# Performance work log

Hardware: AMD Instinct MI355X
Metric: run time of the kernel (lower is better)

The kernel has to match this reference:

```python
import jax, jax.numpy as jnp
import numpy as np

DECAY = 0.99
EPS = 1e-05
B, T, DIM, N_EMBED = 64, 1024, 256, 1024


def setup_inputs() -> dict:
    key = jax.random.key(0)
    k1, k2 = jax.random.split(key, 2)
    input_ = jax.random.normal(k1, (B, T, DIM), dtype=jnp.float32)
    embed = jax.random.normal(k2, (DIM, N_EMBED), dtype=jnp.float32)  # buffer 'embed'
    cluster_size = jnp.zeros((N_EMBED,), dtype=jnp.float32)           # buffer 'cluster_size'
    embed_avg = embed.copy()                                          # buffer 'embed_avg'
    return {"input_": input_, "embed": embed, "cluster_size": cluster_size, "embed_avg": embed_avg}


def reference(input_, embed, cluster_size, embed_avg):
    n_embed = embed.shape[1]
    flatten = input_.reshape(-1, embed.shape[0])  # [N, dim]
    dist = (jnp.sum(flatten * flatten, axis=-1, keepdims=True)
            - 2.0 * flatten @ embed
            + jnp.sum(embed * embed, axis=0, keepdims=True))
    embed_ind = jnp.argmin(dist, axis=1)  # (-dist).max(1) == argmin(dist)
    quantize = jnp.take(embed.T, embed_ind, axis=0).reshape(input_.shape)

    # training-mode EMA codebook update (buffers are detached in torch)
    # embed_onehot_sum = onehot.sum(0); embed_sum = flatten.T @ onehot
    # implemented via segment_sum (same math, no NxK one-hot materialized)
    ones = jnp.ones((flatten.shape[0],), dtype=flatten.dtype)
    embed_onehot_sum = jax.ops.segment_sum(ones, embed_ind, num_segments=n_embed)
    embed_sum = jax.ops.segment_sum(flatten, embed_ind, num_segments=n_embed).T  # [dim, n_embed]

    new_cluster_size = cluster_size * DECAY + (1.0 - DECAY) * embed_onehot_sum
    # NOTE: original code applies .mul_(decay) TWICE to embed_avg -> decay**2 (faithful)
    new_embed_avg = embed_avg * (DECAY * DECAY) + (1.0 - DECAY) * embed_sum
    n = jnp.sum(new_cluster_size)
    cs = (new_cluster_size + EPS) / (n + n_embed * EPS) * n
    new_embed = new_embed_avg / cs[None, :]

    diff = jnp.mean((jax.lax.stop_gradient(quantize) - input_) ** 2)
    quantize_st = input_ + jax.lax.stop_gradient(quantize - input_)
    return quantize_st, diff, embed_ind, new_cluster_size, new_embed_avg, new_embed
```

## Files before the change

kernel.cpp:

```cpp
#include <hip/hip_runtime.h>
#include <float.h>

#define DECAY 0.99f
#define EPS 1e-5f
#define NROWS 65536
#define DIM 256
#define NEMB 1024
#define CH 64
#define MAXSUB 2048

typedef _Float16 f16;
typedef _Float16 half8 __attribute__((ext_vector_type(8)));
typedef float f32x4 __attribute__((ext_vector_type(4)));

__global__ __launch_bounds__(256) void k_enorm(const float* __restrict__ embed,
                                               float* __restrict__ enorm2,
                                               int* __restrict__ counts) {
    int kk = threadIdx.x & 63;
    int dg = threadIdx.x >> 6;
    int k  = blockIdx.x * 64 + kk;
    float s = 0.f;
    for (int d = dg; d < DIM; d += 4) {
        float v = embed[(size_t)d * NEMB + k];
        s = fmaf(v, v, s);
    }
    __shared__ float red[4][64];
    red[dg][kk] = s;
    __syncthreads();
    if (dg == 0) enorm2[k] = red[0][kk] + red[1][kk] + red[2][kk] + red[3][kk];
    int gt = blockIdx.x * 256 + threadIdx.x;
    if (gt < NEMB) counts[gt] = 0;
}

__global__ __launch_bounds__(256) void k_transpose(const float* __restrict__ embed,
                                                   float* __restrict__ embedT) {
    __shared__ float tile[32][33];
    int k0 = blockIdx.x * 32, d0 = blockIdx.y * 32;
    int tx = threadIdx.x, ty = threadIdx.y;
#pragma unroll
    for (int i = 0; i < 4; i++)
        tile[ty + 8 * i][tx] = embed[(size_t)(d0 + ty + 8 * i) * NEMB + k0 + tx];
    __syncthreads();
#pragma unroll
    for (int i = 0; i < 4; i++)
        embedT[(size_t)(k0 + ty + 8 * i) * DIM + d0 + tx] = tile[tx][ty + 8 * i];
}

__global__ __launch_bounds__(256) void k_esplit(const float* __restrict__ embed,
                                                f16* __restrict__ ehlT) {
    __shared__ float tile[32][33];
    int c0 = blockIdx.x * 32, d0 = blockIdx.y * 32;
    int tx = threadIdx.x, ty = threadIdx.y;
#pragma unroll
    for (int i = 0; i < 4; i++)
        tile[ty + 8 * i][tx] = embed[(size_t)(d0 + ty + 8 * i) * NEMB + c0 + tx];
    __syncthreads();
#pragma unroll
    for (int i = 0; i < 4; i++) {
        int c = c0 + ty + 8 * i;
        int d = d0 + tx;
        float v = tile[tx][ty + 8 * i];
        f16 h = (f16)v;
        f16 l = (f16)(v - (float)h);
        ehlT[(size_t)c * 512 + d]       = h;
        ehlT[(size_t)c * 512 + 256 + d] = l;
    }
}

#define LDS_A  0
#define LDS_B  131072
#define LDS_SZ 147456

__global__ __launch_bounds__(512, 2) void k_argmin_mfma(const float* __restrict__ input,
                                                        const f16* __restrict__ ehlT,
                                                        const float* __restrict__ enorm2,
                                                        int* __restrict__ ind,
                                                        float* __restrict__ out_ind) {
    __shared__ char lds[LDS_SZ];
    const int tid  = threadIdx.x;
    const int lane = tid & 63;
    const int w    = tid >> 6;
    const int wr   = w >> 2;
    const int wc   = w & 3;
    const int rb   = blockIdx.x * 128;
    const int l15  = lane & 15;
    const int lkh  = lane >> 4;
    const int swa  = (l15 & 7) << 4;
    const int swb  = ((l15 >> 1) & 3) << 4;

#pragma unroll
    for (int it8 = 0; it8 < 4; it8++) {
        int task = tid + 512 * it8;
        int row = task >> 4, ch = task & 15;
        const float4* g = (const float4*)(input + (size_t)(rb + row) * DIM + ch * 16);
        float fv[16];
        *(float4*)(fv + 0)  = g[0];
        *(float4*)(fv + 4)  = g[1];
        *(float4*)(fv + 8)  = g[2];
        *(float4*)(fv + 12) = g[3];
        half8 hh[2], llv[2];
#pragma unroll
        for (int u = 0; u < 2; u++)
#pragma unroll
            for (int e = 0; e < 8; e++) {
                float x = fv[u * 8 + e];
                f16 h = (f16)x;
                hh[u][e]  = h;
                llv[u][e] = (f16)(x - (float)h);
            }
        int rbase = row * 1024;
        int sw = (row & 7) << 4;
        *(half8*)(lds + LDS_A + rbase + (((ch * 2    ) * 16) ^ sw)) = hh[0];
        *(half8*)(lds + LDS_A + rbase + (((ch * 2 + 1) * 16) ^ sw)) = hh[1];
        *(half8*)(lds + LDS_A + rbase + (((32 + ch * 2) * 16) ^ sw)) = llv[0];
        *(half8*)(lds + LDS_A + rbase + (((33 + ch * 2) * 16) ^ sw)) = llv[1];
    }

#pragma unroll
    for (int u = 0; u < 2; u++) {
        int g = tid + 512 * u;
        int col = g >> 2, s = g & 3;
        half8 h = *(const half8*)(ehlT + (size_t)col * 512 + s * 8);
        *(half8*)(lds + LDS_B + col * 64 + ((s * 16) ^ (((col >> 1) & 3) << 4))) = h;
    }
    __syncthreads();

    float bv[16];
    int   bi[16];
#pragma unroll
    for (int q = 0; q < 16; q++) { bv[q] = FLT_MAX; bi[q] = 0x7fffffff; }

    for (int ct = 0; ct < 4; ct++) {
        const int cb = ct * 256;
        f32x4 acc[4][4];
#pragma unroll
        for (int fr = 0; fr < 4; fr++)
#pragma unroll
            for (int fc = 0; fc < 4; fc++) acc[fr][fc] = (f32x4){0.f, 0.f, 0.f, 0.f};

        for (int kt = 0; kt < 24; kt++) {
            const int it = ct * 24 + kt;
            const bool hn = (it < 95);
            float4 nb0, nb1;
            int wa0 = 0, wa1 = 0;
            if (hn) {
                int itn = it + 1;
                int ct2 = itn / 24;
                int kt2 = itn - ct2 * 24;
                int seg2 = kt2 >> 3, kq2 = kt2 & 7;
                int koff2 = ((seg2 == 2) ? 256 : 0) + kq2 * 32;
                int cb2 = ct2 * 256;
                int g0 = tid, col0 = g0 >> 2, s0 = g0 & 3;
                nb0 = *(const float4*)(ehlT + (size_t)(cb2 + col0) * 512 + koff2 + s0 * 8);
                wa0 = col0 * 64 + ((s0 * 16) ^ (((col0 >> 1) & 3) << 4));
                int g1 = tid + 512, col1 = g1 >> 2, s1 = g1 & 3;
                nb1 = *(const float4*)(ehlT + (size_t)(cb2 + col1) * 512 + koff2 + s1 * 8);
                wa1 = col1 * 64 + ((s1 * 16) ^ (((col1 >> 1) & 3) << 4));
            }
            const int seg = kt >> 3, kq = kt & 7;
            const int abase = ((seg == 1) ? 32 : 0) + kq * 4;
            const int jslot = abase + lkh;
            half8 af[4], bf[4];
#pragma unroll
            for (int f = 0; f < 4; f++) {
                int row = wr * 64 + f * 16 + l15;
                af[f] = *(const half8*)(lds + LDS_A + row * 1024 + ((jslot * 16) ^ swa));
            }
#pragma unroll
            for (int f = 0; f < 4; f++) {
                int col = wc * 64 + f * 16 + l15;
                bf[f] = *(const half8*)(lds + LDS_B + col * 64 + ((lkh * 16) ^ swb));
            }
#pragma unroll
            for (int fr = 0; fr < 4; fr++)
#pragma unroll
                for (int fc = 0; fc < 4; fc++)
                    acc[fr][fc] = __builtin_amdgcn_mfma_f32_16x16x32_f16(
                        af[fr], bf[fc], acc[fr][fc], 0, 0, 0);
            if (kt == 23) {
#pragma unroll
                for (int fc = 0; fc < 4; fc++) {
                    int col = cb + wc * 64 + fc * 16 + l15;
                    float e2 = enorm2[col];
#pragma unroll
                    for (int fr = 0; fr < 4; fr++)
#pragma unroll
                        for (int r = 0; r < 4; r++) {
                            float s = fmaf(-2.f, acc[fr][fc][r], e2);
                            int q = fr * 4 + r;
                            if (s < bv[q]) { bv[q] = s; bi[q] = col; }
                        }
                }
            }
            __syncthreads();
            if (hn) {
                *(half8*)(lds + LDS_B + wa0) = *(half8*)&nb0;
                *(half8*)(lds + LDS_B + wa1) = *(half8*)&nb1;
            }
            __syncthreads();
        }
    }

#pragma unroll
    for (int q = 0; q < 16; q++) {
        float v = bv[q]; int i = bi[q];
#pragma unroll
        for (int m = 1; m <= 8; m <<= 1) {
            float ov = __shfl_xor(v, m, 64);
            int   oi = __shfl_xor(i, m, 64);
            if (ov < v || (ov == v && oi < i)) { v = ov; i = oi; }
        }
        bv[q] = v; bi[q] = i;
    }
    float* PV = (float*)(lds + LDS_B);
    int*   PI = (int*)(lds + LDS_B + 2048);
    if (l15 == 0) {
#pragma unroll
        for (int fr = 0; fr < 4; fr++)
#pragma unroll
            for (int r = 0; r < 4; r++) {
                int rrow = wr * 64 + fr * 16 + lkh * 4 + r;
                PV[rrow * 4 + wc] = bv[fr * 4 + r];
                PI[rrow * 4 + wc] = bi[fr * 4 + r];
            }
    }
    __syncthreads();
    if (tid < 128) {
        float best = FLT_MAX; int bidx = 0x7fffffff;
#pragma unroll
        for (int t = 0; t < 4; t++) {
            float v = PV[tid * 4 + t];
            int   i = PI[tid * 4 + t];
            if (v < best || (v == best && i < bidx)) { best = v; bidx = i; }
        }
        ind[rb + tid] = bidx;
        out_ind[rb + tid] = (float)bidx;
    }
}

__global__ __launch_bounds__(256) void k_quant(const float* __restrict__ input,
                                               const float* __restrict__ embedT,
                                               const int* __restrict__ ind,
                                               float* __restrict__ out_q,
                                               float* __restrict__ partials) {
    const int tid = threadIdx.x;
    const unsigned gid = blockIdx.x * 256 + tid;
    float s = 0.f;
#pragma unroll
    for (int j = 0; j < 8; j++) {
        size_t i4 = (size_t)gid + (size_t)j * 524288u;
        int row = (int)(i4 >> 6);
        int d4  = (int)(i4 & 63);
        float4 iv = *reinterpret_cast<const float4*>(input + i4 * 4);
        int k = ind[row];
        float4 qv = *reinterpret_cast<const float4*>(embedT + (size_t)k * DIM + d4 * 4);
        float dx = qv.x - iv.x, dy = qv.y - iv.y, dz = qv.z - iv.z, dw = qv.w - iv.w;
        float4 ov;
        ov.x = iv.x + dx; ov.y = iv.y + dy; ov.z = iv.z + dz; ov.w = iv.w + dw;
        *reinterpret_cast<float4*>(out_q + i4 * 4) = ov;
        s += dx * dx + dy * dy + dz * dz + dw * dw;
    }
    __shared__ float red[256];
    red[tid] = s;
    __syncthreads();
    for (int off = 128; off > 0; off >>= 1) {
        if (tid < off) red[tid] += red[tid + off];
        __syncthreads();
    }
    if (tid == 0) partials[blockIdx.x] = red[0];
}

__global__ __launch_bounds__(256) void k_diff(const float* __restrict__ partials,
                                              float* __restrict__ out_diff) {
    __shared__ float red[256];
    int tid = threadIdx.x;
    float s = 0.f;
    for (int j = 0; j < 8; j++) s += partials[tid * 8 + j];
    red[tid] = s;
    __syncthreads();
    for (int off = 128; off > 0; off >>= 1) {
        if (tid < off) red[tid] += red[tid + off];
        __syncthreads();
    }
    if (tid == 0) out_diff[0] = red[0] / 16777216.0f;
}

__global__ __launch_bounds__(256) void k_hist(const int* __restrict__ ind,
                                              int* __restrict__ counts) {
    __shared__ int h[NEMB];
    int tid = threadIdx.x;
    for (int j = tid; j < NEMB; j += 256) h[j] = 0;
    __syncthreads();
    for (int i = blockIdx.x * 256 + tid; i < NROWS; i += 64 * 256)
        atomicAdd(&h[ind[i]], 1);
    __syncthreads();
    for (int j = tid; j < NEMB; j += 256)
        if (h[j]) atomicAdd(&counts[j], h[j]);
}

__global__ __launch_bounds__(1024) void k_scan(const int* __restrict__ counts,
                                               const float* __restrict__ cluster_size,
                                               int* __restrict__ offsets,
                                               int* __restrict__ cursor,
                                               int* __restrict__ substart,
                                               float* __restrict__ out_ncs,
                                               float* __restrict__ cs) {
    __shared__ int sh[NEMB];
    __shared__ float shf[NEMB];
    int tid = threadIdx.x;
    int c = counts[tid];
    sh[tid] = c;
    __syncthreads();
    for (int off = 1; off < NEMB; off <<= 1) {
        int t = (tid >= off) ? sh[tid - off] : 0;
        __syncthreads();
        sh[tid] += t;
        __syncthreads();
    }
    int excl = sh[tid] - c;
    offsets[tid] = excl;
    cursor[tid]  = excl;
    int sc = (c + CH - 1) / CH;
    __syncthreads();
    sh[tid] = sc;
    __syncthreads();
    for (int off = 1; off < NEMB; off <<= 1) {
        int t = (tid >= off) ? sh[tid - off] : 0;
        __syncthreads();
        sh[tid] += t;
        __syncthreads();
    }
    substart[tid] = sh[tid] - sc;
    if (tid == NEMB - 1) substart[NEMB] = sh[tid];
    float ncs = cluster_size[tid] * DECAY + (1.f - DECAY) * (float)c;
    out_ncs[tid] = ncs;
    shf[tid] = ncs;
    __syncthreads();
    for (int off = 512; off > 0; off >>= 1) {
        if (tid < off) shf[tid] += shf[tid + off];
        __syncthreads();
    }
    float n = shf[0];
    cs[tid] = (ncs + EPS) / (n + NEMB * EPS) * n;
}

__global__ __launch_bounds__(256) void k_scatter(const int* __restrict__ ind,
                                                 int* __restrict__ cursor,
                                                 int* __restrict__ sorted) {
    int i = blockIdx.x * 256 + threadIdx.x;
    int k = ind[i];
    int pos = atomicAdd(&cursor[k], 1);
    sorted[pos] = i;
}

__global__ __launch_bounds__(256) void k_psum(const float* __restrict__ input,
                                              const int* __restrict__ sorted,
                                              const int* __restrict__ counts,
                                              const int* __restrict__ offsets,
                                              const int* __restrict__ substart,
                                              float* __restrict__ partial) {
    const int b = blockIdx.x;
    if (b >= substart[NEMB]) return;
    int lo = 0, hi = NEMB;
    while (hi - lo > 1) {
        int mid = (lo + hi) >> 1;
        if (substart[mid] <= b) lo = mid; else hi = mid;
    }
    const int k     = lo;
    const int chunk = b - substart[k];
    const int cnt   = counts[k];
    const int base  = offsets[k] + chunk * CH;
    const int lim   = min(CH, cnt - chunk * CH);
    const int d     = threadIdx.x;
    float s = 0.f;
    for (int i = 0; i < lim; i++) {
        int row = sorted[base + i];
        s += input[(size_t)row * DIM + d];
    }
    partial[(size_t)b * DIM + d] = s;
}

__global__ __launch_bounds__(256) void k_ema(const float* __restrict__ partial,
                                             const float* __restrict__ embed_avg,
                                             const int* __restrict__ substart,
                                             const float* __restrict__ cs,
                                             float* __restrict__ out_navg,
                                             float* __restrict__ out_nembed) {
    const int d = blockIdx.x;
    const int t = threadIdx.x;
#pragma unroll
    for (int i = 0; i < 4; i++) {
        int k = t + 256 * i;
        int s0 = substart[k], s1 = substart[k + 1];
        float s = 0.f;
        for (int sub = s0; sub < s1; sub++)
            s += partial[(size_t)sub * DIM + d];
        float navg = embed_avg[(size_t)d * NEMB + k] * (DECAY * DECAY) + (1.f - DECAY) * s;
        out_navg[(size_t)d * NEMB + k] = navg;
        out_nembed[(size_t)d * NEMB + k] = navg / cs[k];
    }
}

extern "C" void kernel_launch(void* const* d_in, const int* in_sizes, int n_in,
                              void* d_out, int out_size, void* d_ws, size_t ws_size,
                              hipStream_t stream) {
    const float* input        = (const float*)d_in[0];
    const float* embed        = (const float*)d_in[1];
    const float* cluster_size = (const float*)d_in[2];
    const float* embed_avg    = (const float*)d_in[3];

    float* out        = (float*)d_out;
    float* out_q      = out;
    float* out_diff   = out + 16777216;
    float* out_ind    = out + 16777217;
    float* out_ncs    = out + 16842753;
    float* out_navg   = out + 16843777;
    float* out_nembed = out + 17105921;

    char* ws = (char*)d_ws;
    size_t o = 0;
    int*   w_ind      = (int*)(ws + o);   o += (size_t)NROWS * 4;
    float* w_embedT   = (float*)(ws + o); o += (size_t)DIM * NEMB * 4;
    float* w_enorm    = (float*)(ws + o); o += NEMB * 4;
    int*   w_counts   = (int*)(ws + o);   o += NEMB * 4;
    int*   w_offsets  = (int*)(ws + o);   o += NEMB * 4;
    int*   w_cursor   = (int*)(ws + o);   o += NEMB * 4;
    float* w_cs       = (float*)(ws + o); o += NEMB * 4;
    float* w_partials = (float*)(ws + o); o += 2048 * 4;
    int*   w_sorted   = (int*)(ws + o);   o += (size_t)NROWS * 4;
    int*   w_substart = (int*)(ws + o);   o += (NEMB + 4) * 4;
    float* w_partial  = (float*)(ws + o); o += (size_t)MAXSUB * DIM * 4;
    f16*   w_ehlT     = (f16*)(ws + o);   o += (size_t)NEMB * 512 * 2;

    k_enorm<<<16, 256, 0, stream>>>(embed, w_enorm, w_counts);
    k_transpose<<<dim3(32, 8), dim3(32, 8), 0, stream>>>(embed, w_embedT);
    k_esplit<<<dim3(32, 8), dim3(32, 8), 0, stream>>>(embed, w_ehlT);
    k_argmin_mfma<<<NROWS / 128, 512, 0, stream>>>(input, w_ehlT, w_enorm, w_ind, out_ind);
    k_quant<<<2048, 256, 0, stream>>>(input, w_embedT, w_ind, out_q, w_partials);
    k_diff<<<1, 256, 0, stream>>>(w_partials, out_diff);
    k_hist<<<64, 256, 0, stream>>>(w_ind, w_counts);
    k_scan<<<1, 1024, 0, stream>>>(w_counts, cluster_size, w_offsets, w_cursor,
                                   w_substart, out_ncs, w_cs);
    k_scatter<<<NROWS / 256, 256, 0, stream>>>(w_ind, w_cursor, w_sorted);
    k_psum<<<MAXSUB, 256, 0, stream>>>(input, w_sorted, w_counts, w_offsets,
                                       w_substart, w_partial);
    k_ema<<<DIM, 256, 0, stream>>>(w_partial, embed_avg, w_substart, w_cs,
                                   out_navg, out_nembed);
}
```

Before: 306.5 us.

## Double-buffer codebook tiles via direct global-to-LDS loads and fuse prep kernels

Replaces the register-staged codebook tile copy in the argmin MFMA kernel with global_load_lds direct loads into two alternating LDS buffers. This removes one of the two barriers per k-step and the round trip through registers. The swizzle is moved into the global address pattern so the LDS layout stays the same. The transpose and fp16 hi/lo split kernels are also merged into one launch, and LDS use rises by 16KB per block, which could affect occupancy at two blocks per CU.

```diff
diff --git a/kernel.cpp b/kernel.cpp
--- a/kernel.cpp
+++ b/kernel.cpp
@@ -8,6 +8,9 @@
 #define NEMB 1024
 #define CH 64
 #define MAXSUB 2048
+
+#define GLOBAL_AS __attribute__((address_space(1)))
+#define LOCAL_AS  __attribute__((address_space(3)))
 
 typedef _Float16 f16;
 typedef _Float16 half8 __attribute__((ext_vector_type(8)));
@@ -32,22 +35,9 @@
     if (gt < NEMB) counts[gt] = 0;
 }
 
-__global__ __launch_bounds__(256) void k_transpose(const float* __restrict__ embed,
-                                                   float* __restrict__ embedT) {
-    __shared__ float tile[32][33];
-    int k0 = blockIdx.x * 32, d0 = blockIdx.y * 32;
-    int tx = threadIdx.x, ty = threadIdx.y;
-#pragma unroll
-    for (int i = 0; i < 4; i++)
-        tile[ty + 8 * i][tx] = embed[(size_t)(d0 + ty + 8 * i) * NEMB + k0 + tx];
-    __syncthreads();
-#pragma unroll
-    for (int i = 0; i < 4; i++)
-        embedT[(size_t)(k0 + ty + 8 * i) * DIM + d0 + tx] = tile[tx][ty + 8 * i];
-}
-
-__global__ __launch_bounds__(256) void k_esplit(const float* __restrict__ embed,
-                                                f16* __restrict__ ehlT) {
+__global__ __launch_bounds__(256) void k_prep(const float* __restrict__ embed,
+                                              float* __restrict__ embedT,
+                                              f16* __restrict__ ehlT) {
     __shared__ float tile[32][33];
     int c0 = blockIdx.x * 32, d0 = blockIdx.y * 32;
     int tx = threadIdx.x, ty = threadIdx.y;
@@ -60,16 +50,17 @@
         int c = c0 + ty + 8 * i;
         int d = d0 + tx;
         float v = tile[tx][ty + 8 * i];
+        embedT[(size_t)c * DIM + d] = v;
         f16 h = (f16)v;
-        f16 l = (f16)(v - (float)h);
         ehlT[(size_t)c * 512 + d]       = h;
-        ehlT[(size_t)c * 512 + 256 + d] = l;
+        ehlT[(size_t)c * 512 + 256 + d] = (f16)(v - (float)h);
     }
 }
 
 #define LDS_A  0
-#define LDS_B  131072
-#define LDS_SZ 147456
+#define LDS_B0 131072
+#define LDS_B1 147456
+#define LDS_SZ 163840
 
 __global__ __launch_bounds__(512, 2) void k_argmin_mfma(const float* __restrict__ input,
                                                         const f16* __restrict__ ehlT,
@@ -87,6 +78,16 @@
     const int lkh  = lane >> 4;
     const int swa  = (l15 & 7) << 4;
     const int swb  = ((l15 >> 1) & 3) << 4;
+    const int slot_log   = (lane & 3) ^ ((lane >> 3) & 3);
+    const int gl_laneoff = (lane >> 2) * 512 + slot_log * 8;
+
+#pragma unroll
+    for (int i = 0; i < 2; i++) {
+        int chunkid = w * 2 + i;
+        const f16* src = ehlT + (size_t)chunkid * 8192 + gl_laneoff;
+        __builtin_amdgcn_global_load_lds((const GLOBAL_AS unsigned*)src,
+            (LOCAL_AS unsigned*)(lds + LDS_B0 + chunkid * 1024), 16, 0, 0);
+    }
 
 #pragma unroll
     for (int it8 = 0; it8 < 4; it8++) {
@@ -115,14 +116,6 @@
         *(half8*)(lds + LDS_A + rbase + (((32 + ch * 2) * 16) ^ sw)) = llv[0];
         *(half8*)(lds + LDS_A + rbase + (((33 + ch * 2) * 16) ^ sw)) = llv[1];
     }
-
-#pragma unroll
-    for (int u = 0; u < 2; u++) {
-        int g = tid + 512 * u;
-        int col = g >> 2, s = g & 3;
-        half8 h = *(const half8*)(ehlT + (size_t)col * 512 + s * 8);
-        *(half8*)(lds + LDS_B + col * 64 + ((s * 16) ^ (((col >> 1) & 3) << 4))) = h;
-    }
     __syncthreads();
 
     float bv[16];
@@ -130,6 +123,7 @@
 #pragma unroll
     for (int q = 0; q < 16; q++) { bv[q] = FLT_MAX; bi[q] = 0x7fffffff; }
 
+    int p = 0;
     for (int ct = 0; ct < 4; ct++) {
         const int cb = ct * 256;
         f32x4 acc[4][4];
@@ -140,26 +134,25 @@
 
         for (int kt = 0; kt < 24; kt++) {
             const int it = ct * 24 + kt;
-            const bool hn = (it < 95);
-            float4 nb0, nb1;
-            int wa0 = 0, wa1 = 0;
-            if (hn) {
+            if (it < 95) {
                 int itn = it + 1;
                 int ct2 = itn / 24;
                 int kt2 = itn - ct2 * 24;
                 int seg2 = kt2 >> 3, kq2 = kt2 & 7;
                 int koff2 = ((seg2 == 2) ? 256 : 0) + kq2 * 32;
-                int cb2 = ct2 * 256;
-                int g0 = tid, col0 = g0 >> 2, s0 = g0 & 3;
-                nb0 = *(const float4*)(ehlT + (size_t)(cb2 + col0) * 512 + koff2 + s0 * 8);
-                wa0 = col0 * 64 + ((s0 * 16) ^ (((col0 >> 1) & 3) << 4));
-                int g1 = tid + 512, col1 = g1 >> 2, s1 = g1 & 3;
-                nb1 = *(const float4*)(ehlT + (size_t)(cb2 + col1) * 512 + koff2 + s1 * 8);
-                wa1 = col1 * 64 + ((s1 * 16) ^ (((col1 >> 1) & 3) << 4));
+                const f16* base = ehlT + (size_t)ct2 * 131072 + koff2 + gl_laneoff;
+                char* dstb = lds + (p ? LDS_B0 : LDS_B1);
+#pragma unroll
+                for (int i = 0; i < 2; i++) {
+                    int chunkid = w * 2 + i;
+                    __builtin_amdgcn_global_load_lds(
+                        (const GLOBAL_AS unsigned*)(base + (size_t)chunkid * 8192),
+                        (LOCAL_AS unsigned*)(dstb + chunkid * 1024), 16, 0, 0);
+                }
             }
             const int seg = kt >> 3, kq = kt & 7;
-            const int abase = ((seg == 1) ? 32 : 0) + kq * 4;
-            const int jslot = abase + lkh;
+            const int jslot = ((seg == 1) ? 32 : 0) + kq * 4 + lkh;
+            const char* Bb = lds + (p ? LDS_B1 : LDS_B0);
             half8 af[4], bf[4];
 #pragma unroll
             for (int f = 0; f < 4; f++) {
@@ -169,7 +162,7 @@
 #pragma unroll
             for (int f = 0; f < 4; f++) {
                 int col = wc * 64 + f * 16 + l15;
-                bf[f] = *(const half8*)(lds + LDS_B + col * 64 + ((lkh * 16) ^ swb));
+                bf[f] = *(const half8*)(Bb + col * 64 + ((lkh * 16) ^ swb));
             }
 #pragma unroll
             for (int fr = 0; fr < 4; fr++)
@@ -193,11 +186,7 @@
                 }
             }
             __syncthreads();
-            if (hn) {
-                *(half8*)(lds + LDS_B + wa0) = *(half8*)&nb0;
-                *(half8*)(lds + LDS_B + wa1) = *(half8*)&nb1;
-            }
-            __syncthreads();
+            p ^= 1;
         }
     }
 
@@ -212,8 +201,8 @@
         }
         bv[q] = v; bi[q] = i;
     }
-    float* PV = (float*)(lds + LDS_B);
-    int*   PI = (int*)(lds + LDS_B + 2048);
+    float* PV = (float*)(lds + LDS_B0);
+    int*   PI = (int*)(lds + LDS_B0 + 2048);
     if (l15 == 0) {
 #pragma unroll
         for (int fr = 0; fr < 4; fr++)
@@ -433,8 +422,7 @@
     f16*   w_ehlT     = (f16*)(ws + o);   o += (size_t)NEMB * 512 * 2;
 
     k_enorm<<<16, 256, 0, stream>>>(embed, w_enorm, w_counts);
-    k_transpose<<<dim3(32, 8), dim3(32, 8), 0, stream>>>(embed, w_embedT);
-    k_esplit<<<dim3(32, 8), dim3(32, 8), 0, stream>>>(embed, w_ehlT);
+    k_prep<<<dim3(32, 8), dim3(32, 8), 0, stream>>>(embed, w_embedT, w_ehlT);
     k_argmin_mfma<<<NROWS / 128, 512, 0, stream>>>(input, w_ehlT, w_enorm, w_ind, out_ind);
     k_quant<<<2048, 256, 0, stream>>>(input, w_embedT, w_ind, out_q, w_partials);
     k_diff<<<1, 256, 0, stream>>>(w_partials, out_diff);
```

New measurement: 294.2 us. -4.0%, faster.
